# Optimization experiments

Hardware: AMD Instinct MI355X
Metric: run time of the kernel (lower is better)

## Reference

```python
import jax, jax.numpy as jnp
import numpy as np

B, S, D = 2, 2048, 2048
H, KV, HD = 32, 8, 64
REP = H // KV  # 4


def setup_inputs() -> dict:
    key = jax.random.key(0)
    ks = jax.random.split(key, 5)
    x = jax.random.normal(ks[0], (B, S, D), jnp.float32)
    # Llama rope frequencies: theta=10000, pairs of adjacent dims
    inv_freq = 1.0 / (10000.0 ** (np.arange(0, HD, 2, dtype=np.float64) / HD))  # [HD/2]
    ang = np.outer(np.arange(S, dtype=np.float64), inv_freq)  # [S, HD/2]
    freqs_cis = jnp.asarray(np.stack([np.cos(ang), np.sin(ang)], axis=-1), jnp.float32)  # [S, HD/2, 2]
    wq = jax.random.normal(ks[1], (H * HD, D), jnp.float32) * 0.02
    wk = jax.random.normal(ks[2], (KV * HD, D), jnp.float32) * 0.02
    wv = jax.random.normal(ks[3], (KV * HD, D), jnp.float32) * 0.02
    wo = jax.random.normal(ks[4], (D, H * HD), jnp.float32) * 0.02
    return {"x": x, "freqs_cis": freqs_cis, "wq": wq, "wk": wk, "wv": wv, "wo": wo}


def _apply_rope(t, cos, sin):
    # t: [B,S,nh,HD]; cos/sin: [S,HD/2]; complex multiply on adjacent pairs
    b, s, nh, hd = t.shape
    t2 = t.reshape(b, s, nh, hd // 2, 2)
    tr, ti = t2[..., 0], t2[..., 1]
    c = cos[None, :, None, :]
    sn = sin[None, :, None, :]
    out = jnp.stack([tr * c - ti * sn, tr * sn + ti * c], axis=-1)
    return out.reshape(b, s, nh, hd)


def reference(x, freqs_cis, wq, wk, wv, wo):
    # QKV projections (torch Linear: y = x @ W.T)
    q = jnp.einsum('bsd,ed->bse', x, wq).reshape(B, S, H, HD)
    k = jnp.einsum('bsd,ed->bse', x, wk).reshape(B, S, KV, HD)
    v = jnp.einsum('bsd,ed->bse', x, wv).reshape(B, S, KV, HD)
    cos, sin = freqs_cis[..., 0], freqs_cis[..., 1]
    q = _apply_rope(q, cos, sin)
    k = _apply_rope(k, cos, sin)
    # GQA without materializing repeated K/V: group query heads by KV head
    qg = q.reshape(B, S, KV, REP, HD)
    scale = 1.0 / jnp.sqrt(jnp.asarray(HD, q.dtype))
    scores = jnp.einsum('bsgrd,btgd->bgrst', qg, k) * scale  # [B,KV,REP,S,S]
    causal = jnp.tril(jnp.ones((S, S), bool))
    scores = jnp.where(causal, scores, -jnp.inf)
    p = jax.nn.softmax(scores, axis=-1)
    o = jnp.einsum('bgrst,btgd->bsgrd', p, v).reshape(B, S, H * HD)
    return jnp.einsum('bse,de->bsd', o, wo)
```

## Files before the change

### kernel.cpp

```cpp
#include <hip/hip_runtime.h>
#include <cstdint>
#include <cstddef>

#define B_ 2
#define S_ 2048
#define D_ 2048
#define H_ 32
#define KV_ 8
#define HD_ 64
#define M_ (B_*S_)
#define EQ_ (H_*HD_)
#define EK_ (KV_*HD_)

typedef unsigned short u16;
typedef __attribute__((ext_vector_type(8))) short s16x8;
typedef __attribute__((ext_vector_type(4))) float f32x4;

#define QSCALE 0.18033688011112042f
#define EXPOFF 15.869645449778564f

#if __has_builtin(__builtin_amdgcn_exp2f)
#define EXP2(x) __builtin_amdgcn_exp2f(x)
#else
#define EXP2(x) __expf((x) * 0.6931471805599453f)
#endif

__device__ __forceinline__ u16 f2bf(float f) {
  unsigned u = __float_as_uint(f);
  u += 0x7fffu + ((u >> 16) & 1u);
  return (u16)(u >> 16);
}
__device__ __forceinline__ unsigned pk2(float a, float b) {
  unsigned ua = __float_as_uint(a) + 0x8000u;
  unsigned ub = __float_as_uint(b) + 0x8000u;
  return __builtin_amdgcn_perm(ub, ua, 0x07060302);
}
__device__ __forceinline__ f32x4 mfma16(s16x8 a, s16x8 b, f32x4 c) {
  return __builtin_amdgcn_mfma_f32_16x16x32_bf16(a, b, c, 0, 0, 0);
}
__device__ __forceinline__ void gl_lds16(const void* g, void* l) {
  __builtin_amdgcn_global_load_lds(
      (const __attribute__((address_space(1))) void*)g,
      (__attribute__((address_space(3))) void*)l, 16, 0, 0);
}

__global__ void cast_all(const float4* __restrict__ x, const float4* __restrict__ wq,
                         const float4* __restrict__ wk, const float4* __restrict__ wv,
                         const float4* __restrict__ wo, ushort4* __restrict__ dst) {
  int i = blockIdx.x * 256 + threadIdx.x;
  const float4* src; int off;
  if (i < 2097152)      { src = x;  off = i; }
  else if (i < 3145728) { src = wq; off = i - 2097152; }
  else if (i < 3407872) { src = wk; off = i - 3145728; }
  else if (i < 3670016) { src = wv; off = i - 3407872; }
  else                  { src = wo; off = i - 3670016; }
  float4 v = src[off];
  ushort4 r;
  r.x = f2bf(v.x); r.y = f2bf(v.y); r.z = f2bf(v.z); r.w = f2bf(v.w);
  dst[i] = r;
}

__global__ __launch_bounds__(256)
void gemm_qkv(const u16* __restrict__ A, const u16* __restrict__ Bw,
              u16* __restrict__ qb, u16* __restrict__ kb, u16* __restrict__ vtb,
              const float* __restrict__ fc) {
  __shared__ __align__(16) u16 As[2][128 * 32];
  __shared__ __align__(16) u16 Bs[2][96 * 32];
  const int tid  = threadIdx.x;
  const int lane = tid & 63;
  const int wave = tid >> 6;
  const int m0 = blockIdx.y * 128;
  const int n0 = blockIdx.x * 96;
  const int wm = (wave >> 1) * 64;
  const int wn = (wave & 1) * 48;
  const int l15 = lane & 15;
  const int quad = lane >> 4;

  const int ca0 = tid,      ra0 = ca0 >> 2, pa0 = ca0 & 3;
  const int ca1 = tid + 256, ra1 = ca1 >> 2, pa1 = ca1 & 3;
  const int cb0 = tid,      rb0 = cb0 >> 2, pb0 = cb0 & 3;
  const int cb1 = tid + 256, rb1 = cb1 >> 2, pb1 = cb1 & 3;
  const u16* Ap0 = A + (size_t)(m0 + ra0) * D_ + (pa0 ^ ((ra0 >> 1) & 3)) * 8;
  const u16* Ap1 = A + (size_t)(m0 + ra1) * D_ + (pa1 ^ ((ra1 >> 1) & 3)) * 8;
  const u16* Bp0 = Bw + (size_t)(n0 + rb0) * D_ + (pb0 ^ ((rb0 >> 1) & 3)) * 8;
  const u16* Bp1 = Bw + (size_t)(n0 + rb1) * D_ + (pb1 ^ ((rb1 >> 1) & 3)) * 8;
  const bool doB1 = (tid < 128);

  f32x4 acc[4][3] = {};

  gl_lds16(Ap0, &As[0][ca0 * 8]);
  gl_lds16(Ap1, &As[0][ca1 * 8]);
  gl_lds16(Bp0, &Bs[0][cb0 * 8]);
  if (doB1) gl_lds16(Bp1, &Bs[0][cb1 * 8]);
  __syncthreads();

  for (int ks = 0; ks < 64; ++ks) {
    if (ks + 1 < 64) {
      const int nb = (ks + 1) & 1;
      const int ko = (ks + 1) * 32;
      gl_lds16(Ap0 + ko, &As[nb][ca0 * 8]);
      gl_lds16(Ap1 + ko, &As[nb][ca1 * 8]);
      gl_lds16(Bp0 + ko, &Bs[nb][cb0 * 8]);
      if (doB1) gl_lds16(Bp1 + ko, &Bs[nb][cb1 * 8]);
    }

    const u16* as = &As[ks & 1][0];
    const u16* bs = &Bs[ks & 1][0];
    s16x8 af[4], bfr[3];
    #pragma unroll
    for (int mi = 0; mi < 4; ++mi) {
      int row = wm + mi * 16 + l15;
      af[mi] = *(const s16x8*)&as[row * 32 + (quad ^ ((row >> 1) & 3)) * 8];
    }
    #pragma unroll
    for (int ni = 0; ni < 3; ++ni) {
      int row = wn + ni * 16 + l15;
      bfr[ni] = *(const s16x8*)&bs[row * 32 + (quad ^ ((row >> 1) & 3)) * 8];
    }
    #pragma unroll
    for (int mi = 0; mi < 4; ++mi)
      #pragma unroll
      for (int ni = 0; ni < 3; ++ni)
        acc[mi][ni] = mfma16(af[mi], bfr[ni], acc[mi][ni]);

    __syncthreads();
  }

  const float sg = (l15 & 1) ? 1.f : -1.f;
  #pragma unroll
  for (int mi = 0; mi < 4; ++mi) {
    #pragma unroll
    for (int ni = 0; ni < 3; ++ni) {
      const int col = n0 + wn + ni * 16 + l15;
      if (col < 2560) {
        const bool isQ = (col < 2048);
        u16* dst = isQ ? qb : kb;
        const int ncol0 = isQ ? 0 : 2048;
        const int ndim  = isQ ? EQ_ : EK_;
        const float scale = isQ ? QSCALE : 1.0f;
        const int ip = (col & 63) >> 1;
        #pragma unroll
        for (int r = 0; r < 4; ++r) {
          int row = m0 + wm + mi * 16 + quad * 4 + r;
          const float* fr = fc + (size_t)(row & (S_ - 1)) * 64;
          float c  = fr[ip * 2];
          float sn = fr[ip * 2 + 1];
          float v = acc[mi][ni][r];
          float p = __shfl_xor(v, 1, 64);
          float o = (v * c + sg * (p * sn)) * scale;
          dst[(size_t)row * ndim + col - ncol0] = f2bf(o);
        }
      } else {
        const int vcol = col - 2560;
        uint2 w;
        w.x = pk2(acc[mi][ni][0], acc[mi][ni][1]);
        w.y = pk2(acc[mi][ni][2], acc[mi][ni][3]);
        *(uint2*)(vtb + (size_t)vcol * M_ + m0 + wm + mi * 16 + quad * 4) = w;
      }
    }
  }
}

__global__ __launch_bounds__(256)
void gemm_o(const u16* __restrict__ A, const u16* __restrict__ Bw, float* __restrict__ C,
            int Ndim, int Kdim) {
  __shared__ __align__(16) u16 As[2][64 * 32];
  __shared__ __align__(16) u16 Bs[2][128 * 32];
  const int tid  = threadIdx.x;
  const int lane = tid & 63;
  const int wave = tid >> 6;
  const int m0 = blockIdx.y * 64;
  const int n0 = blockIdx.x * 128;
  const int wm = (wave >> 1) * 32;
  const int wn = (wave & 1) * 64;
  const int l15 = lane & 15;
  const int quad = lane >> 4;

  const int ca0 = tid,      ra0 = ca0 >> 2, pa0 = ca0 & 3;
  const int cb0 = tid,      rb0 = cb0 >> 2, pb0 = cb0 & 3;
  const int cb1 = tid + 256, rb1 = cb1 >> 2, pb1 = cb1 & 3;
  const u16* Ap0 = A + (size_t)(m0 + ra0) * Kdim + (pa0 ^ ((ra0 >> 1) & 3)) * 8;
  const u16* Bp0 = Bw + (size_t)(n0 + rb0) * Kdim + (pb0 ^ ((rb0 >> 1) & 3)) * 8;
  const u16* Bp1 = Bw + (size_t)(n0 + rb1) * Kdim + (pb1 ^ ((rb1 >> 1) & 3)) * 8;

  f32x4 acc[2][4] = {};

  const int nsteps = Kdim >> 5;

  gl_lds16(Ap0, &As[0][ca0 * 8]);
  gl_lds16(Bp0, &Bs[0][cb0 * 8]);
  gl_lds16(Bp1, &Bs[0][cb1 * 8]);
  __syncthreads();

  for (int ks = 0; ks < nsteps; ++ks) {
    if (ks + 1 < nsteps) {
      const int nb = (ks + 1) & 1;
      const int ko = (ks + 1) * 32;
      gl_lds16(Ap0 + ko, &As[nb][ca0 * 8]);
      gl_lds16(Bp0 + ko, &Bs[nb][cb0 * 8]);
      gl_lds16(Bp1 + ko, &Bs[nb][cb1 * 8]);
    }

    const u16* as = &As[ks & 1][0];
    const u16* bs = &Bs[ks & 1][0];
    s16x8 af[2], bfr[4];
    #pragma unroll
    for (int mi = 0; mi < 2; ++mi) {
      int row = wm + mi * 16 + l15;
      af[mi] = *(const s16x8*)&as[row * 32 + (quad ^ ((row >> 1) & 3)) * 8];
    }
    #pragma unroll
    for (int ni = 0; ni < 4; ++ni) {
      int row = wn + ni * 16 + l15;
      bfr[ni] = *(const s16x8*)&bs[row * 32 + (quad ^ ((row >> 1) & 3)) * 8];
    }
    #pragma unroll
    for (int mi = 0; mi < 2; ++mi)
      #pragma unroll
      for (int ni = 0; ni < 4; ++ni)
        acc[mi][ni] = mfma16(af[mi], bfr[ni], acc[mi][ni]);

    __syncthreads();
  }

  #pragma unroll
  for (int mi = 0; mi < 2; ++mi) {
    #pragma unroll
    for (int r = 0; r < 4; ++r) {
      int row = m0 + wm + mi * 16 + quad * 4 + r;
      size_t base = (size_t)row * Ndim + n0 + wn;
      #pragma unroll
      for (int ni = 0; ni < 4; ++ni)
        C[base + ni * 16 + l15] = acc[mi][ni][r];
    }
  }
}

__global__ __launch_bounds__(256, 4)
void flash_attn(const u16* __restrict__ qb, const u16* __restrict__ kb,
                const u16* __restrict__ vtb, u16* __restrict__ ob) {
  const int bx = blockIdx.x;
  const int h  = blockIdx.y;
  const int b  = blockIdx.z;
  const int g  = h >> 2;
  const int tid  = threadIdx.x;
  const int lane = tid & 63;
  const int wave = tid >> 6;
  const int l15  = lane & 15;
  const int quad = lane >> 4;
  const int kq   = quad * 8;

  const int Tlo = bx, Thi = 31 - bx;
  const int n_lo = Tlo + 1, n_hi = Thi + 1;
  const int rL = Tlo * 64 + wave * 16;
  const int rH = Thi * 64 + wave * 16;
  const int rowL = rL + l15;
  const int rowH = rH + l15;

  __shared__ __align__(16) u16 Ks[2][8 * 512];
  __shared__ __align__(16) u16 Vs[2][8 * 512];
  __shared__ __align__(16) u16 Pl[4][16 * 64];

  char* Pb = (char*)&Pl[wave][0];
  const int pm = (l15 & 7) << 4;

  const u16* qpL = qb + (size_t)(b * S_ + rL + l15) * EQ_ + h * HD_;
  const u16* qpH = qb + (size_t)(b * S_ + rH + l15) * EQ_ + h * HD_;
  s16x8 qL0 = *(const s16x8*)(qpL + kq);
  s16x8 qL1 = *(const s16x8*)(qpL + 32 + kq);
  s16x8 qH0 = *(const s16x8*)(qpH + kq);
  s16x8 qH1 = *(const s16x8*)(qpH + 32 + kq);

  f32x4 OL[4] = {}, OH[4] = {};
  float sumL = 0.f, sumH = 0.f;

  const int sw = wave & 1;
  const bool doK = (wave < 2);

  const u16* stbase;
  size_t     tstride;
  if (doK) {
    stbase  = kb + (size_t)(b * S_ + lane) * EK_ + g * HD_ + sw * 32;
    tstride = (size_t)64 * EK_;
  } else {
    stbase  = vtb + (size_t)(g * HD_ + lane) * M_ + b * S_ + sw * 32;
    tstride = 64;
  }
  const int ldoff = sw * 4 * 512 + lane * 8;
  u16* mybuf0 = (doK ? &Ks[0][0] : &Vs[0][0]) + ldoff;
  u16* mybuf1 = (doK ? &Ks[1][0] : &Vs[1][0]) + ldoff;

  #pragma unroll
  for (int r = 0; r < 4; ++r)
    gl_lds16(stbase + r * 8, mybuf0 + r * 512);
  __syncthreads();

  for (int kt = 0; kt < n_hi; ++kt) {
    const int t0 = kt * 64;
    const u16* kcur = &Ks[kt & 1][0];
    const u16* vcur = &Vs[kt & 1][0];

    if (kt + 1 < n_hi) {
      const u16* src = stbase + (size_t)(kt + 1) * tstride;
      u16* dst = ((kt + 1) & 1) ? mybuf1 : mybuf0;
      #pragma unroll
      for (int r = 0; r < 4; ++r)
        gl_lds16(src + r * 8, dst + r * 512);
    }

    const bool do_lo = (kt < n_lo);
    const bool mH = (kt == n_hi - 1);
    const bool mL = (kt == n_lo - 1);

    s16x8 kk0[4], kk1[4];
    #pragma unroll
    for (int ts = 0; ts < 4; ++ts) {
      kk0[ts] = *(const s16x8*)&kcur[quad * 512 + (ts * 16 + l15) * 8];
      kk1[ts] = *(const s16x8*)&kcur[(4 + quad) * 512 + (ts * 16 + l15) * 8];
    }

    #pragma unroll
    for (int ts = 0; ts < 4; ++ts) {
      const int tb = t0 + ts * 16 + quad * 4;
      f32x4 s = {};
      s = mfma16(kk0[ts], qH0, s);
      s = mfma16(kk1[ts], qH1, s);
      if (mH) {
        #pragma unroll
        for (int r = 0; r < 4; ++r) if (tb + r > rowH) s[r] = -1e30f;
      }
      float p0 = EXP2(s[0] - EXPOFF), p1 = EXP2(s[1] - EXPOFF);
      float p2 = EXP2(s[2] - EXPOFF), p3 = EXP2(s[3] - EXPOFF);
      sumH += (p0 + p1) + (p2 + p3);
      uint2 w; w.x = pk2(p0, p1); w.y = pk2(p2, p3);
      *(uint2*)(Pb + l15 * 128 + ((ts * 32 + quad * 8) ^ pm)) = w;
    }
    s16x8 pH0 = *(const s16x8*)(Pb + l15 * 128 + ((quad * 16) ^ pm));
    s16x8 pH1 = *(const s16x8*)(Pb + l15 * 128 + ((64 + quad * 16) ^ pm));

    s16x8 pL0 = {}, pL1 = {};
    if (do_lo) {
      #pragma unroll
      for (int ts = 0; ts < 4; ++ts) {
        const int tb = t0 + ts * 16 + quad * 4;
        f32x4 s = {};
        s = mfma16(kk0[ts], qL0, s);
        s = mfma16(kk1[ts], qL1, s);
        if (mL) {
          #pragma unroll
          for (int r = 0; r < 4; ++r) if (tb + r > rowL) s[r] = -1e30f;
        }
        float p0 = EXP2(s[0] - EXPOFF), p1 = EXP2(s[1] - EXPOFF);
        float p2 = EXP2(s[2] - EXPOFF), p3 = EXP2(s[3] - EXPOFF);
        sumL += (p0 + p1) + (p2 + p3);
        uint2 w; w.x = pk2(p0, p1); w.y = pk2(p2, p3);
        *(uint2*)(Pb + l15 * 128 + ((ts * 32 + quad * 8) ^ pm)) = w;
      }
      pL0 = *(const s16x8*)(Pb + l15 * 128 + ((quad * 16) ^ pm));
      pL1 = *(const s16x8*)(Pb + l15 * 128 + ((64 + quad * 16) ^ pm));
    }

    #pragma unroll
    for (int df = 0; df < 4; ++df) {
      s16x8 v0 = *(const s16x8*)&vcur[quad * 512 + (df * 16 + l15) * 8];
      s16x8 v1 = *(const s16x8*)&vcur[(4 + quad) * 512 + (df * 16 + l15) * 8];
      OH[df] = mfma16(v1, pH1, mfma16(v0, pH0, OH[df]));
      if (do_lo) OL[df] = mfma16(v1, pL1, mfma16(v0, pL0, OL[df]));
    }

    __syncthreads();
  }

  sumH += __shfl_xor(sumH, 16, 64); sumH += __shfl_xor(sumH, 32, 64);
  sumL += __shfl_xor(sumL, 16, 64); sumL += __shfl_xor(sumL, 32, 64);
  float invH = 1.f / sumH, invL = 1.f / sumL;

  {
    u16* op = ob + (size_t)(b * S_ + rowH) * EQ_ + h * HD_;
    #pragma unroll
    for (int df = 0; df < 4; ++df) {
      uint2 w;
      w.x = pk2(OH[df][0] * invH, OH[df][1] * invH);
      w.y = pk2(OH[df][2] * invH, OH[df][3] * invH);
      *(uint2*)(op + df * 16 + quad * 4) = w;
    }
  }
  {
    u16* op = ob + (size_t)(b * S_ + rowL) * EQ_ + h * HD_;
    #pragma unroll
    for (int df = 0; df < 4; ++df) {
      uint2 w;
      w.x = pk2(OL[df][0] * invL, OL[df][1] * invL);
      w.y = pk2(OL[df][2] * invL, OL[df][3] * invL);
      *(uint2*)(op + df * 16 + quad * 4) = w;
    }
  }
}

extern "C" void kernel_launch(void* const* d_in, const int* in_sizes, int n_in,
                              void* d_out, int out_size, void* d_ws, size_t ws_size,
                              hipStream_t stream) {
  (void)in_sizes; (void)n_in; (void)out_size; (void)ws_size;
  const float* x  = (const float*)d_in[0];
  const float* fc = (const float*)d_in[1];
  const float* wq = (const float*)d_in[2];
  const float* wk = (const float*)d_in[3];
  const float* wv = (const float*)d_in[4];
  const float* wo = (const float*)d_in[5];
  float* out = (float*)d_out;
  char* ws = (char*)d_ws;

  u16* xb  = (u16*)(ws);
  u16* wqb = (u16*)(ws + 16777216);
  u16* wob = (u16*)(ws + 29360128);
  u16* qb  = (u16*)(ws + 37748736);
  u16* kb  = (u16*)(ws + 54525952);
  u16* vtb = (u16*)(ws + 58720256);
  u16* ob  = (u16*)(ws + 62914560);

  cast_all<<<18432, 256, 0, stream>>>((const float4*)x, (const float4*)wq,
                                      (const float4*)wk, (const float4*)wv,
                                      (const float4*)wo, (ushort4*)ws);

  gemm_qkv<<<dim3(32, 32), 256, 0, stream>>>(xb, wqb, qb, kb, vtb, fc);

  flash_attn<<<dim3(16, 32, 2), 256, 0, stream>>>(qb, kb, vtb, ob);

  gemm_o<<<dim3(16, 64), 256, 0, stream>>>(ob, wob, out, D_, EQ_);
}
```

Before: 310.1 us.

## Keep softmax probabilities in registers by permuting K row load order

Permutes the key rows loaded into shared memory so the QK^T MFMA output layout lines up with the B-operand layout needed for the PV MFMA. The probabilities can then be packed straight into registers instead of round-tripping through a per-wave LDS scratch buffer. This removes LDS writes and reads per tile and frees shared memory, at the cost of more live registers and a remapped causal-mask index.

After: 317.2 us. 1.02x slower.

```diff
diff --git a/kernel.cpp b/kernel.cpp
--- a/kernel.cpp
+++ b/kernel.cpp
@@ -259,10 +259,6 @@
 
   __shared__ __align__(16) u16 Ks[2][8 * 512];
   __shared__ __align__(16) u16 Vs[2][8 * 512];
-  __shared__ __align__(16) u16 Pl[4][16 * 64];
-
-  char* Pb = (char*)&Pl[wave][0];
-  const int pm = (l15 & 7) << 4;
 
   const u16* qpL = qb + (size_t)(b * S_ + rL + l15) * EQ_ + h * HD_;
   const u16* qpH = qb + (size_t)(b * S_ + rH + l15) * EQ_ + h * HD_;
@@ -277,10 +273,12 @@
   const int sw = wave & 1;
   const bool doK = (wave < 2);
 
+  const int tl = (lane & 0x23) | ((lane & 0x0C) << 1) | ((lane & 0x10) >> 2);
+
   const u16* stbase;
   size_t     tstride;
   if (doK) {
-    stbase  = kb + (size_t)(b * S_ + lane) * EK_ + g * HD_ + sw * 32;
+    stbase  = kb + (size_t)(b * S_ + tl) * EK_ + g * HD_ + sw * 32;
     tstride = (size_t)64 * EK_;
   } else {
     stbase  = vtb + (size_t)(g * HD_ + lane) * M_ + b * S_ + sw * 32;
@@ -295,6 +293,8 @@
     gl_lds16(stbase + r * 8, mybuf0 + r * 512);
   __syncthreads();
 
+  union PU { s16x8 v; unsigned u[4]; };
+
   for (int kt = 0; kt < n_hi; ++kt) {
     const int t0 = kt * 64;
     const u16* kcur = &Ks[kt & 1][0];
@@ -319,53 +319,79 @@
       kk1[ts] = *(const s16x8*)&kcur[(4 + quad) * 512 + (ts * 16 + l15) * 8];
     }
 
-    #pragma unroll
-    for (int ts = 0; ts < 4; ++ts) {
-      const int tb = t0 + ts * 16 + quad * 4;
-      f32x4 s = {};
-      s = mfma16(kk0[ts], qH0, s);
-      s = mfma16(kk1[ts], qH1, s);
+    PU pH0u, pH1u;
+    {
+      f32x4 sH[4];
+      #pragma unroll
+      for (int ts = 0; ts < 4; ++ts) {
+        f32x4 s = {};
+        s = mfma16(kk0[ts], qH0, s);
+        s = mfma16(kk1[ts], qH1, s);
+        sH[ts] = s;
+      }
       if (mH) {
         #pragma unroll
-        for (int r = 0; r < 4; ++r) if (tb + r > rowH) s[r] = -1e30f;
+        for (int ts = 0; ts < 4; ++ts) {
+          const int tb = t0 + ((ts & 2) << 4) + ((ts & 1) << 2) + quad * 8;
+          #pragma unroll
+          for (int r = 0; r < 4; ++r) if (tb + r > rowH) sH[ts][r] = -1e30f;
+        }
       }
-      float p0 = EXP2(s[0] - EXPOFF), p1 = EXP2(s[1] - EXPOFF);
-      float p2 = EXP2(s[2] - EXPOFF), p3 = EXP2(s[3] - EXPOFF);
-      sumH += (p0 + p1) + (p2 + p3);
-      uint2 w; w.x = pk2(p0, p1); w.y = pk2(p2, p3);
-      *(uint2*)(Pb + l15 * 128 + ((ts * 32 + quad * 8) ^ pm)) = w;
-    }
-    s16x8 pH0 = *(const s16x8*)(Pb + l15 * 128 + ((quad * 16) ^ pm));
-    s16x8 pH1 = *(const s16x8*)(Pb + l15 * 128 + ((64 + quad * 16) ^ pm));
-
-    s16x8 pL0 = {}, pL1 = {};
+      float e[16];
+      #pragma unroll
+      for (int ts = 0; ts < 4; ++ts)
+        #pragma unroll
+        for (int r = 0; r < 4; ++r) {
+          float x = EXP2(sH[ts][r] - EXPOFF);
+          e[ts * 4 + r] = x;
+          sumH += x;
+        }
+      pH0u.u[0] = pk2(e[0],  e[1]);  pH0u.u[1] = pk2(e[2],  e[3]);
+      pH0u.u[2] = pk2(e[4],  e[5]);  pH0u.u[3] = pk2(e[6],  e[7]);
+      pH1u.u[0] = pk2(e[8],  e[9]);  pH1u.u[1] = pk2(e[10], e[11]);
+      pH1u.u[2] = pk2(e[12], e[13]); pH1u.u[3] = pk2(e[14], e[15]);
+    }
+
+    PU pL0u, pL1u;
+    pL0u.v = s16x8{}; pL1u.v = s16x8{};
     if (do_lo) {
+      f32x4 sL[4];
       #pragma unroll
       for (int ts = 0; ts < 4; ++ts) {
-        const int tb = t0 + ts * 16 + quad * 4;
         f32x4 s = {};
         s = mfma16(kk0[ts], qL0, s);
         s = mfma16(kk1[ts], qL1, s);
-        if (mL) {
+        sL[ts] = s;
+      }
+      if (mL) {
+        #pragma unroll
+        for (int ts = 0; ts < 4; ++ts) {
+          const int tb = t0 + ((ts & 2) << 4) + ((ts & 1) << 2) + quad * 8;
           #pragma unroll
-          for (int r = 0; r < 4; ++r) if (tb + r > rowL) s[r] = -1e30f;
+          for (int r = 0; r < 4; ++r) if (tb + r > rowL) sL[ts][r] = -1e30f;
         }
-        float p0 = EXP2(s[0] - EXPOFF), p1 = EXP2(s[1] - EXPOFF);
-        float p2 = EXP2(s[2] - EXPOFF), p3 = EXP2(s[3] - EXPOFF);
-        sumL += (p0 + p1) + (p2 + p3);
-        uint2 w; w.x = pk2(p0, p1); w.y = pk2(p2, p3);
-        *(uint2*)(Pb + l15 * 128 + ((ts * 32 + quad * 8) ^ pm)) = w;
       }
-      pL0 = *(const s16x8*)(Pb + l15 * 128 + ((quad * 16) ^ pm));
-      pL1 = *(const s16x8*)(Pb + l15 * 128 + ((64 + quad * 16) ^ pm));
+      float e[16];
+      #pragma unroll
+      for (int ts = 0; ts < 4; ++ts)
+        #pragma unroll
+        for (int r = 0; r < 4; ++r) {
+          float x = EXP2(sL[ts][r] - EXPOFF);
+          e[ts * 4 + r] = x;
+          sumL += x;
+        }
+      pL0u.u[0] = pk2(e[0],  e[1]);  pL0u.u[1] = pk2(e[2],  e[3]);
+      pL0u.u[2] = pk2(e[4],  e[5]);  pL0u.u[3] = pk2(e[6],  e[7]);
+      pL1u.u[0] = pk2(e[8],  e[9]);  pL1u.u[1] = pk2(e[10], e[11]);
+      pL1u.u[2] = pk2(e[12], e[13]); pL1u.u[3] = pk2(e[14], e[15]);
     }
 
     #pragma unroll
     for (int df = 0; df < 4; ++df) {
       s16x8 v0 = *(const s16x8*)&vcur[quad * 512 + (df * 16 + l15) * 8];
       s16x8 v1 = *(const s16x8*)&vcur[(4 + quad) * 512 + (df * 16 + l15) * 8];
-      OH[df] = mfma16(v1, pH1, mfma16(v0, pH0, OH[df]));
-      if (do_lo) OL[df] = mfma16(v1, pL1, mfma16(v0, pL0, OL[df]));
+      OH[df] = mfma16(v1, pH1u.v, mfma16(v0, pH0u.v, OH[df]));
+      if (do_lo) OL[df] = mfma16(v1, pL1u.v, mfma16(v0, pL0u.v, OL[df]));
     }
 
     __syncthreads();
```

## Process two query heads per attention block and keep P in registers

Applied to the files above, without the earlier changes.

Each flash attention block now handles two query heads that share a KV group, so every K/V tile loaded into LDS is reused for twice as many heads and the grid is halved. The LDS round-trip for the probability matrix is removed. K rows are loaded in a permuted order so the QK MFMA output layout already matches the B-operand layout needed by the PV MFMA, and the probabilities are packed straight from registers. The cost is many more live registers (four accumulator sets and eight Q fragments), handled by lowering launch bounds occupancy from 4 to 2, which reduces latency hiding.

Result: faster. 285.8 us (-7.8%).

```diff
diff --git a/kernel.cpp b/kernel.cpp
--- a/kernel.cpp
+++ b/kernel.cpp
@@ -236,13 +236,52 @@
   }
 }
 
-__global__ __launch_bounds__(256, 4)
+__device__ __forceinline__ void qk_pass(const s16x8* kk0, const s16x8* kk1,
+                                        s16x8 q0, s16x8 q1, bool msk, int rowX,
+                                        int t0, int quad, float& sum,
+                                        s16x8& p0v, s16x8& p1v) {
+  union PU { s16x8 v; unsigned u[4]; };
+  f32x4 sS[4];
+  #pragma unroll
+  for (int ts = 0; ts < 4; ++ts) {
+    f32x4 s = {};
+    s = mfma16(kk0[ts], q0, s);
+    s = mfma16(kk1[ts], q1, s);
+    sS[ts] = s;
+  }
+  if (msk) {
+    #pragma unroll
+    for (int ts = 0; ts < 4; ++ts) {
+      const int tb = t0 + ((ts & 2) << 4) + ((ts & 1) << 2) + quad * 8;
+      #pragma unroll
+      for (int r = 0; r < 4; ++r) if (tb + r > rowX) sS[ts][r] = -1e30f;
+    }
+  }
+  float e[16];
+  #pragma unroll
+  for (int ts = 0; ts < 4; ++ts)
+    #pragma unroll
+    for (int r = 0; r < 4; ++r) {
+      float x = EXP2(sS[ts][r] - EXPOFF);
+      e[ts * 4 + r] = x;
+      sum += x;
+    }
+  PU p0u, p1u;
+  p0u.u[0] = pk2(e[0],  e[1]);  p0u.u[1] = pk2(e[2],  e[3]);
+  p0u.u[2] = pk2(e[4],  e[5]);  p0u.u[3] = pk2(e[6],  e[7]);
+  p1u.u[0] = pk2(e[8],  e[9]);  p1u.u[1] = pk2(e[10], e[11]);
+  p1u.u[2] = pk2(e[12], e[13]); p1u.u[3] = pk2(e[14], e[15]);
+  p0v = p0u.v; p1v = p1u.v;
+}
+
+__global__ __launch_bounds__(256, 2)
 void flash_attn(const u16* __restrict__ qb, const u16* __restrict__ kb,
                 const u16* __restrict__ vtb, u16* __restrict__ ob) {
   const int bx = blockIdx.x;
-  const int h  = blockIdx.y;
+  const int hy = blockIdx.y;
   const int b  = blockIdx.z;
-  const int g  = h >> 2;
+  const int h0 = hy * 2;
+  const int g  = hy >> 1;
   const int tid  = threadIdx.x;
   const int lane = tid & 63;
   const int wave = tid >> 6;
@@ -259,28 +298,30 @@
 
   __shared__ __align__(16) u16 Ks[2][8 * 512];
   __shared__ __align__(16) u16 Vs[2][8 * 512];
-  __shared__ __align__(16) u16 Pl[4][16 * 64];
-
-  char* Pb = (char*)&Pl[wave][0];
-  const int pm = (l15 & 7) << 4;
-
-  const u16* qpL = qb + (size_t)(b * S_ + rL + l15) * EQ_ + h * HD_;
-  const u16* qpH = qb + (size_t)(b * S_ + rH + l15) * EQ_ + h * HD_;
-  s16x8 qL0 = *(const s16x8*)(qpL + kq);
-  s16x8 qL1 = *(const s16x8*)(qpL + 32 + kq);
-  s16x8 qH0 = *(const s16x8*)(qpH + kq);
-  s16x8 qH1 = *(const s16x8*)(qpH + 32 + kq);
-
-  f32x4 OL[4] = {}, OH[4] = {};
-  float sumL = 0.f, sumH = 0.f;
+
+  const u16* qpH0 = qb + (size_t)(b * S_ + rH + l15) * EQ_ + h0 * HD_;
+  const u16* qpL0 = qb + (size_t)(b * S_ + rL + l15) * EQ_ + h0 * HD_;
+  s16x8 qHa0 = *(const s16x8*)(qpH0 + kq);
+  s16x8 qHa1 = *(const s16x8*)(qpH0 + 32 + kq);
+  s16x8 qHb0 = *(const s16x8*)(qpH0 + HD_ + kq);
+  s16x8 qHb1 = *(const s16x8*)(qpH0 + HD_ + 32 + kq);
+  s16x8 qLa0 = *(const s16x8*)(qpL0 + kq);
+  s16x8 qLa1 = *(const s16x8*)(qpL0 + 32 + kq);
+  s16x8 qLb0 = *(const s16x8*)(qpL0 + HD_ + kq);
+  s16x8 qLb1 = *(const s16x8*)(qpL0 + HD_ + 32 + kq);
+
+  f32x4 OHa[4] = {}, OHb[4] = {}, OLa[4] = {}, OLb[4] = {};
+  float sumHa = 0.f, sumHb = 0.f, sumLa = 0.f, sumLb = 0.f;
 
   const int sw = wave & 1;
   const bool doK = (wave < 2);
+
+  const int tl = (lane & 0x23) | ((lane & 0x0C) << 1) | ((lane & 0x10) >> 2);
 
   const u16* stbase;
   size_t     tstride;
   if (doK) {
-    stbase  = kb + (size_t)(b * S_ + lane) * EK_ + g * HD_ + sw * 32;
+    stbase  = kb + (size_t)(b * S_ + tl) * EK_ + g * HD_ + sw * 32;
     tstride = (size_t)64 * EK_;
   } else {
     stbase  = vtb + (size_t)(g * HD_ + lane) * M_ + b * S_ + sw * 32;
@@ -319,80 +360,64 @@
       kk1[ts] = *(const s16x8*)&kcur[(4 + quad) * 512 + (ts * 16 + l15) * 8];
     }
 
-    #pragma unroll
-    for (int ts = 0; ts < 4; ++ts) {
-      const int tb = t0 + ts * 16 + quad * 4;
-      f32x4 s = {};
-      s = mfma16(kk0[ts], qH0, s);
-      s = mfma16(kk1[ts], qH1, s);
-      if (mH) {
-        #pragma unroll
-        for (int r = 0; r < 4; ++r) if (tb + r > rowH) s[r] = -1e30f;
-      }
-      float p0 = EXP2(s[0] - EXPOFF), p1 = EXP2(s[1] - EXPOFF);
-      float p2 = EXP2(s[2] - EXPOFF), p3 = EXP2(s[3] - EXPOFF);
-      sumH += (p0 + p1) + (p2 + p3);
-      uint2 w; w.x = pk2(p0, p1); w.y = pk2(p2, p3);
-      *(uint2*)(Pb + l15 * 128 + ((ts * 32 + quad * 8) ^ pm)) = w;
-    }
-    s16x8 pH0 = *(const s16x8*)(Pb + l15 * 128 + ((quad * 16) ^ pm));
-    s16x8 pH1 = *(const s16x8*)(Pb + l15 * 128 + ((64 + quad * 16) ^ pm));
-
-    s16x8 pL0 = {}, pL1 = {};
+    s16x8 pHa0, pHa1, pHb0, pHb1, pLa0, pLa1, pLb0, pLb1;
+    qk_pass(kk0, kk1, qHa0, qHa1, mH, rowH, t0, quad, sumHa, pHa0, pHa1);
+    qk_pass(kk0, kk1, qHb0, qHb1, mH, rowH, t0, quad, sumHb, pHb0, pHb1);
     if (do_lo) {
-      #pragma unroll
-      for (int ts = 0; ts < 4; ++ts) {
-        const int tb = t0 + ts * 16 + quad * 4;
-        f32x4 s = {};
-        s = mfma16(kk0[ts], qL0, s);
-        s = mfma16(kk1[ts], qL1, s);
-        if (mL) {
-          #pragma unroll
-          for (int r = 0; r < 4; ++r) if (tb + r > rowL) s[r] = -1e30f;
-        }
-        float p0 = EXP2(s[0] - EXPOFF), p1 = EXP2(s[1] - EXPOFF);
-        float p2 = EXP2(s[2] - EXPOFF), p3 = EXP2(s[3] - EXPOFF);
-        sumL += (p0 + p1) + (p2 + p3);
-        uint2 w; w.x = pk2(p0, p1); w.y = pk2(p2, p3);
-        *(uint2*)(Pb + l15 * 128 + ((ts * 32 + quad * 8) ^ pm)) = w;
-      }
-      pL0 = *(const s16x8*)(Pb + l15 * 128 + ((quad * 16) ^ pm));
-      pL1 = *(const s16x8*)(Pb + l15 * 128 + ((64 + quad * 16) ^ pm));
+      qk_pass(kk0, kk1, qLa0, qLa1, mL, rowL, t0, quad, sumLa, pLa0, pLa1);
+      qk_pass(kk0, kk1, qLb0, qLb1, mL, rowL, t0, quad, sumLb, pLb0, pLb1);
+    } else {
+      pLa0 = s16x8{}; pLa1 = s16x8{}; pLb0 = s16x8{}; pLb1 = s16x8{};
     }
 
     #pragma unroll
     for (int df = 0; df < 4; ++df) {
       s16x8 v0 = *(const s16x8*)&vcur[quad * 512 + (df * 16 + l15) * 8];
       s16x8 v1 = *(const s16x8*)&vcur[(4 + quad) * 512 + (df * 16 + l15) * 8];
-      OH[df] = mfma16(v1, pH1, mfma16(v0, pH0, OH[df]));
-      if (do_lo) OL[df] = mfma16(v1, pL1, mfma16(v0, pL0, OL[df]));
+      OHa[df] = mfma16(v1, pHa1, mfma16(v0, pHa0, OHa[df]));
+      OHb[df] = mfma16(v1, pHb1, mfma16(v0, pHb0, OHb[df]));
+      if (do_lo) {
+        OLa[df] = mfma16(v1, pLa1, mfma16(v0, pLa0, OLa[df]));
+        OLb[df] = mfma16(v1, pLb1, mfma16(v0, pLb0, OLb[df]));
+      }
     }
 
     __syncthreads();
   }
 
-  sumH += __shfl_xor(sumH, 16, 64); sumH += __shfl_xor(sumH, 32, 64);
-  sumL += __shfl_xor(sumL, 16, 64); sumL += __shfl_xor(sumL, 32, 64);
-  float invH = 1.f / sumH, invL = 1.f / sumL;
+  sumHa += __shfl_xor(sumHa, 16, 64); sumHa += __shfl_xor(sumHa, 32, 64);
+  sumHb += __shfl_xor(sumHb, 16, 64); sumHb += __shfl_xor(sumHb, 32, 64);
+  sumLa += __shfl_xor(sumLa, 16, 64); sumLa += __shfl_xor(sumLa, 32, 64);
+  sumLb += __shfl_xor(sumLb, 16, 64); sumLb += __shfl_xor(sumLb, 32, 64);
+  float iHa = 1.f / sumHa, iHb = 1.f / sumHb;
+  float iLa = 1.f / sumLa, iLb = 1.f / sumLb;
 
   {
-    u16* op = ob + (size_t)(b * S_ + rowH) * EQ_ + h * HD_;
+    u16* op = ob + (size_t)(b * S_ + rowH) * EQ_ + h0 * HD_;
     #pragma unroll
     for (int df = 0; df < 4; ++df) {
       uint2 w;
-      w.x = pk2(OH[df][0] * invH, OH[df][1] * invH);
-      w.y = pk2(OH[df][2] * invH, OH[df][3] * invH);
+      w.x = pk2(OHa[df][0] * iHa, OHa[df][1] * iHa);
+      w.y = pk2(OHa[df][2] * iHa, OHa[df][3] * iHa);
       *(uint2*)(op + df * 16 + quad * 4) = w;
+      uint2 w2;
+      w2.x = pk2(OHb[df][0] * iHb, OHb[df][1] * iHb);
+      w2.y = pk2(OHb[df][2] * iHb, OHb[df][3] * iHb);
+      *(uint2*)(op + HD_ + df * 16 + quad * 4) = w2;
     }
   }
   {
-    u16* op = ob + (size_t)(b * S_ + rowL) * EQ_ + h * HD_;
+    u16* op = ob + (size_t)(b * S_ + rowL) * EQ_ + h0 * HD_;
     #pragma unroll
     for (int df = 0; df < 4; ++df) {
       uint2 w;
-      w.x = pk2(OL[df][0] * invL, OL[df][1] * invL);
-      w.y = pk2(OL[df][2] * invL, OL[df][3] * invL);
+      w.x = pk2(OLa[df][0] * iLa, OLa[df][1] * iLa);
+      w.y = pk2(OLa[df][2] * iLa, OLa[df][3] * iLa);
       *(uint2*)(op + df * 16 + quad * 4) = w;
+      uint2 w2;
+      w2.x = pk2(OLb[df][0] * iLb, OLb[df][1] * iLb);
+      w2.y = pk2(OLb[df][2] * iLb, OLb[df][3] * iLb);
+      *(uint2*)(op + HD_ + df * 16 + quad * 4) = w2;
     }
   }
 }
@@ -424,7 +449,7 @@
 
   gemm_qkv<<<dim3(32, 32), 256, 0, stream>>>(xb, wqb, qb, kb, vtb, fc);
 
-  flash_attn<<<dim3(16, 32, 2), 256, 0, stream>>>(qb, kb, vtb, ob);
+  flash_attn<<<dim3(16, 16, 2), 256, 0, stream>>>(qb, kb, vtb, ob);
 
   gemm_o<<<dim3(16, 64), 256, 0, stream>>>(ob, wob, out, D_, EQ_);
 }
```
